# Performance work log

Measured on AMD Instinct MI355X. Metric: run time of the kernel, lower is better.

Reference implementation:

```python
import jax, jax.numpy as jnp
import numpy as np

N_NODES = 100000
N_EDGES = 300000
FEAT = 256
N_GRAPHS = 500
N_LAYERS = 6


def setup_inputs() -> dict:
    key = jax.random.key(0)
    ks = jax.random.split(key, 8)
    x = jax.random.normal(ks[0], (N_NODES, FEAT), dtype=jnp.float32)
    edge_index = jax.random.randint(ks[1], (2, N_EDGES), 0, N_NODES, dtype=jnp.int64)
    batch = jnp.sort(jax.random.randint(ks[2], (N_NODES,), 0, N_GRAPHS, dtype=jnp.int64))
    s = 1.0 / np.sqrt(FEAT)
    # PyG SAGEConv params: lin_l (neighbor path, with bias), lin_r (root path, no bias)
    Wl = jax.random.uniform(ks[3], (N_LAYERS, FEAT, FEAT), jnp.float32, -s, s)
    bl = jax.random.uniform(ks[4], (N_LAYERS, FEAT), jnp.float32, -s, s)
    Wr = jax.random.uniform(ks[5], (N_LAYERS, FEAT, FEAT), jnp.float32, -s, s)
    t = jnp.ones((1,), dtype=jnp.float32)  # SoftmaxAggregation learnable temperature, init 1.0
    return {"x": x, "edge_index": edge_index, "batch": batch,
            "Wl": Wl, "bl": bl, "Wr": Wr, "t": t}


def _sage_conv(x, src, dst, Wl, bl, Wr):
    # mean-aggregate source features onto destinations, then lin_l(agg) + lin_r(x)
    msg_sum = jax.ops.segment_sum(x[src], dst, num_segments=N_NODES)  # [N, F]
    deg = jax.ops.segment_sum(jnp.ones((src.shape[0],), x.dtype), dst, num_segments=N_NODES)
    mean = msg_sum / jnp.maximum(deg, 1.0)[:, None]
    return mean @ Wl.T + bl + x @ Wr.T


def _segment_softmax_aggr(x, batch, t):
    # SoftmaxAggregation: alpha = softmax(t*x over nodes per graph, per feature); out = sum(alpha*x)
    s = t * x  # [N, F]
    m = jax.ops.segment_max(s, batch, num_segments=N_GRAPHS)
    m = jnp.where(jnp.isfinite(m), m, 0.0)  # guard empty segments
    e = jnp.exp(s - m[batch])
    denom = jax.ops.segment_sum(e, batch, num_segments=N_GRAPHS)
    alpha = e / jnp.maximum(denom[batch], 1e-16)
    return jax.ops.segment_sum(alpha * x, batch, num_segments=N_GRAPHS)  # [G, F]


def reference(x, edge_index, batch, Wl, bl, Wr, t):
    src, dst = edge_index[0], edge_index[1]
    for i in range(N_LAYERS):
        x = jax.nn.relu(_sage_conv(x, src, dst, Wl[i], bl[i], Wr[i])) + x
    out = _segment_softmax_aggr(x, batch, t[0])
    return out.reshape(-1, FEAT)
```

## Files before the change

kernel.cpp:

```cpp
#include <hip/hip_runtime.h>
#include <hip/hip_bf16.h>

#define N_NODES  100000
#define N_EDGES  300000
#define FEAT     256
#define N_GRAPHS 500
#define N_LAYERS 6
#define SCAN_B   1024

typedef __attribute__((ext_vector_type(8))) short v8s;
typedef __attribute__((ext_vector_type(4))) float v4f;

__device__ __forceinline__ unsigned short f2bf(float f) {
    unsigned u = __float_as_uint(f);
    unsigned r = u + 0x7fffu + ((u >> 16) & 1u);
    return (unsigned short)(r >> 16);
}
__device__ __forceinline__ float bf2f(unsigned short b) {
    return __uint_as_float(((unsigned)b) << 16);
}

__device__ __forceinline__ void gload16(const ushort* g, ushort* l) {
    __builtin_amdgcn_global_load_lds((const __attribute__((address_space(1))) void*)g,
                                     (__attribute__((address_space(3))) void*)l,
                                     16, 0, 0);
}

__global__ __launch_bounds__(256) void init_kernel(const float* __restrict__ x,
                                                   ushort* __restrict__ xb) {
    int i = blockIdx.x * 256 + threadIdx.x;
    if ((size_t)i * 4 >= (size_t)N_NODES * FEAT) return;
    float4 v = ((const float4*)x)[i];
    ((ushort4*)xb)[i] = make_ushort4(f2bf(v.x), f2bf(v.y), f2bf(v.z), f2bf(v.w));
}

__global__ __launch_bounds__(256) void wconv_kernel(const float* __restrict__ Wl,
                                                    const float* __restrict__ Wr,
                                                    ushort* __restrict__ wlb,
                                                    ushort* __restrict__ wrb) {
    int i = blockIdx.x * 256 + threadIdx.x;
    if ((size_t)i * 4 >= (size_t)N_LAYERS * FEAT * FEAT) return;
    float4 a = ((const float4*)Wl)[i];
    float4 b = ((const float4*)Wr)[i];
    ((ushort4*)wlb)[i] = make_ushort4(f2bf(a.x), f2bf(a.y), f2bf(a.z), f2bf(a.w));
    ((ushort4*)wrb)[i] = make_ushort4(f2bf(b.x), f2bf(b.y), f2bf(b.z), f2bf(b.w));
}


__global__ __launch_bounds__(256) void hist_kernel(const int* __restrict__ dst,
                                                   unsigned* __restrict__ degu) {
    int e = blockIdx.x * 256 + threadIdx.x;
    if (e < N_EDGES) atomicAdd(&degu[dst[e]], 1u);
}

__global__ __launch_bounds__(SCAN_B) void scan_blocks(const unsigned* __restrict__ degu,
                                                      unsigned* __restrict__ excl,
                                                      unsigned* __restrict__ bsum) {
    __shared__ unsigned tmp[SCAN_B];
    int i = blockIdx.x * SCAN_B + threadIdx.x;
    unsigned v = (i < N_NODES) ? degu[i] : 0u;
    tmp[threadIdx.x] = v;
    __syncthreads();
    for (int off = 1; off < SCAN_B; off <<= 1) {
        unsigned add = (threadIdx.x >= off) ? tmp[threadIdx.x - off] : 0u;
        __syncthreads();
        tmp[threadIdx.x] += add;
        __syncthreads();
    }
    if (i < N_NODES) excl[i] = tmp[threadIdx.x] - v;
    if (threadIdx.x == SCAN_B - 1) bsum[blockIdx.x] = tmp[SCAN_B - 1];
}

__global__ void scan_tops(unsigned* __restrict__ bsum, int nb) {
    unsigned run = 0;
    for (int b = 0; b < nb; ++b) { unsigned t = bsum[b]; bsum[b] = run; run += t; }
}

__global__ __launch_bounds__(256) void finalize_rowptr(const unsigned* __restrict__ excl,
                                                       const unsigned* __restrict__ bsum,
                                                       unsigned* __restrict__ rowptr,
                                                       unsigned* __restrict__ cursor) {
    int i = blockIdx.x * 256 + threadIdx.x;
    if (i < N_NODES) {
        unsigned v = excl[i] + bsum[i / SCAN_B];
        rowptr[i] = v;
        cursor[i] = v;
    }
    if (i == N_NODES) rowptr[N_NODES] = N_EDGES;
}

__global__ __launch_bounds__(256) void scatter_kernel(const int* __restrict__ ei,
                                                      unsigned* __restrict__ cursor,
                                                      unsigned* __restrict__ col) {
    int e = blockIdx.x * 256 + threadIdx.x;
    if (e >= N_EDGES) return;
    int d = ei[N_EDGES + e];
    unsigned p = atomicAdd(&cursor[d], 1u);
    col[p] = (unsigned)ei[e];
}

__global__ __launch_bounds__(256) void bounds_kernel(const int* __restrict__ batch,
                                                     unsigned* __restrict__ gs,
                                                     unsigned* __restrict__ ge) {
    int i = blockIdx.x * 256 + threadIdx.x;
    if (i >= N_NODES) return;
    int g = batch[i];
    int gp = (i == 0) ? -1 : batch[i - 1];
    if (g != gp) gs[g] = (unsigned)i;
    int gn = (i == N_NODES - 1) ? -1 : batch[i + 1];
    if (g != gn) ge[g] = (unsigned)(i + 1);
}

__global__ __launch_bounds__(256) void agg_csr(const unsigned* __restrict__ rowptr,
                                               const unsigned* __restrict__ col,
                                               const ushort* __restrict__ xb,
                                               ushort* __restrict__ meanb) {
    int node = blockIdx.x * 4 + (threadIdx.x >> 6);
    int lane = threadIdx.x & 63;
    if (node >= N_NODES) return;
    unsigned s = rowptr[node], e = rowptr[node + 1];
    float a0 = 0.f, a1 = 0.f, a2 = 0.f, a3 = 0.f;
    for (unsigned j = s; j < e; ++j) {
        unsigned src = col[j];
        ushort4 v = *(const ushort4*)(xb + (size_t)src * FEAT + lane * 4);
        a0 += bf2f(v.x); a1 += bf2f(v.y); a2 += bf2f(v.z); a3 += bf2f(v.w);
    }
    float r = 1.0f / fmaxf((float)(e - s), 1.0f);
    ushort4 o = make_ushort4(f2bf(a0 * r), f2bf(a1 * r), f2bf(a2 * r), f2bf(a3 * r));
    *(ushort4*)(meanb + (size_t)node * FEAT + lane * 4) = o;
}

#define ATILE 4096
#define BTILE 8192
#define CPAD  264

__global__ __launch_bounds__(512) void gemm_kernel(const ushort* __restrict__ A0,
                                                   const ushort* __restrict__ A1,
                                                   const ushort* __restrict__ B0,
                                                   const ushort* __restrict__ B1,
                                                   const float* __restrict__ bias,
                                                   ushort* __restrict__ xbn) {
    __shared__ ushort lds[36864];
    ushort (*As)[ATILE] = (ushort(*)[ATILE])lds;
    ushort (*Bs)[BTILE] = (ushort(*)[BTILE])(lds + 3 * ATILE);
    ushort* Cs = lds;

    const int tid  = threadIdx.x;
    const int lane = tid & 63;
    const int wid  = tid >> 6;
    const int wr   = wid >> 2;
    const int wc   = wid & 3;
    const int row0 = blockIdx.x * 128;

    v4f acc[4][4] = {};

    const int fr  = lane & 15;
    const int cbk = (lane >> 4) << 4;

    const int pA  = tid >> 3;
    const int w0A = ((tid & 7) ^ (pA & 7)) << 4;
    int rA = row0 + 2 * pA + (w0A >> 6);
    rA = rA < N_NODES ? rA : N_NODES - 1;
    const int cbA = w0A & 63;
    const int pB0  = tid >> 3;
    const int w0B0 = ((tid & 7) ^ (pB0 & 7)) << 4;
    const int rB0  = 2 * pB0 + (w0B0 >> 6);
    const int cbB0 = w0B0 & 63;
    const int c1   = tid + 512;
    const int pB1  = c1 >> 3;
    const int w0B1 = ((c1 & 7) ^ (pB1 & 7)) << 4;
    const int rB1  = 2 * pB1 + (w0B1 >> 6);
    const int cbB1 = w0B1 & 63;

    #define STAGE(buf, kt) do {                                                   \
        const ushort* Asrc = ((kt) < 8) ? A0 : A1;                                \
        const ushort* Bsrc = ((kt) < 8) ? B0 : B1;                                \
        const int kb = ((kt) & 7) * 32;                                           \
        gload16(Asrc + (size_t)rA  * FEAT + kb + (cbA  >> 1), &As[buf][tid * 8]); \
        gload16(Bsrc + (size_t)rB0 * FEAT + kb + (cbB0 >> 1), &Bs[buf][tid * 8]); \
        gload16(Bsrc + (size_t)rB1 * FEAT + kb + (cbB1 >> 1), &Bs[buf][(size_t)c1 * 8]); \
    } while (0)

    #define FRAG(basePtr, row) \
        (*(const v8s*)((const char*)(basePtr) + (((row) >> 1) * 128 + \
            ((((row) & 1) << 6) + cbk) ^ ((((row) >> 1) & 7) << 4))))

    #define DSREAD(buf) do {                                                      \
        _Pragma("unroll")                                                         \
        for (int i = 0; i < 4; ++i) a[i] = FRAG(As[buf], wr * 64 + i * 16 + fr);  \
        _Pragma("unroll")                                                         \
        for (int j = 0; j < 4; ++j) b[j] = FRAG(Bs[buf], wc * 64 + j * 16 + fr);  \
    } while (0)

    #define MFMA16() do {                                                         \
        _Pragma("unroll")                                                         \
        for (int i = 0; i < 4; ++i)                                               \
            _Pragma("unroll")                                                     \
            for (int j = 0; j < 4; ++j)                                           \
                acc[i][j] = __builtin_amdgcn_mfma_f32_16x16x32_bf16(a[i], b[j], acc[i][j], 0, 0, 0); \
    } while (0)

    STAGE(0, 0);
    STAGE(1, 1);
    int bufC = 0, bufS = 2;
    v8s a[4], b[4];
    #pragma unroll 1
    for (int kt = 0; kt < 15; ++kt) {
        asm volatile("s_waitcnt vmcnt(3)" ::: "memory");
        __builtin_amdgcn_s_barrier();
        __builtin_amdgcn_sched_barrier(0);
        if (kt <= 13) STAGE(bufS, kt + 2);
        DSREAD(bufC);
        asm volatile("s_waitcnt lgkmcnt(0)" ::: "memory");
        __builtin_amdgcn_sched_barrier(0);
        __builtin_amdgcn_s_setprio(1);
        MFMA16();
        __builtin_amdgcn_s_setprio(0);
        bufC = (bufC == 2) ? 0 : bufC + 1;
        bufS = (bufS == 2) ? 0 : bufS + 1;
    }
    asm volatile("s_waitcnt vmcnt(0)" ::: "memory");
    __builtin_amdgcn_s_barrier();
    __builtin_amdgcn_sched_barrier(0);
    DSREAD(bufC);
    asm volatile("s_waitcnt lgkmcnt(0)" ::: "memory");
    __builtin_amdgcn_sched_barrier(0);
    MFMA16();

    __builtin_amdgcn_s_barrier();
    {
        const int orow = (lane >> 4) * 4;
        const int ocol = lane & 15;
        #pragma unroll
        for (int j = 0; j < 4; ++j) {
            int colg = wc * 64 + j * 16 + ocol;
            float bv = bias[colg];
            #pragma unroll
            for (int i = 0; i < 4; ++i) {
                int rl = wr * 64 + i * 16 + orow;
                #pragma unroll
                for (int r = 0; r < 4; ++r)
                    Cs[(rl + r) * CPAD + colg] = f2bf(fmaxf(acc[i][j][r] + bv, 0.0f));
            }
        }
    }
    __builtin_amdgcn_s_barrier();
    #pragma unroll
    for (int p = 0; p < 2; ++p) {
        int rl  = p * 64 + (tid >> 3);
        int row = row0 + rl;
        #pragma unroll
        for (int it = 0; it < 4; ++it) {
            int c0 = (tid & 7) * 8 + it * 64;
            v8s y = *(const v8s*)(Cs + rl * CPAD + c0);
            if (row < N_NODES) {
                v8s xv = *(const v8s*)(A1 + (size_t)row * FEAT + c0);
                v8s o;
                #pragma unroll
                for (int k = 0; k < 8; ++k)
                    o[k] = (short)f2bf(bf2f((ushort)y[k]) + bf2f((ushort)xv[k]));
                *(v8s*)(xbn + (size_t)row * FEAT + c0) = o;
            }
        }
    }
    #undef STAGE
    #undef FRAG
    #undef DSREAD
    #undef MFMA16
}

__global__ __launch_bounds__(512) void smax_kernel(const ushort* __restrict__ xb,
                                                   const unsigned* __restrict__ gs,
                                                   const unsigned* __restrict__ ge,
                                                   const float* __restrict__ t,
                                                   float* __restrict__ out) {
    __shared__ float sm[16 * 256];
    __shared__ float sd[16 * 256];
    __shared__ float sa[16 * 256];
    const int g   = blockIdx.x;
    const unsigned s = gs[g], e = ge[g];
    const float tv2 = t[0] * 1.44269504f;
    const int tid = threadIdx.x;
    const int c   = tid >> 5;
    const int f8  = (tid & 31) * 8;

    float m[8], den[8], acc[8];
    #pragma unroll
    for (int k = 0; k < 8; ++k) { m[k] = -INFINITY; den[k] = 0.f; acc[k] = 0.f; }

    if (s < e) {
        for (unsigned n = s + c; n < e; n += 16) {
            v8s v = *(const v8s*)(xb + (size_t)n * FEAT + f8);
            #pragma unroll
            for (int k = 0; k < 8; ++k) {
                float xv = bf2f((ushort)v[k]);
                float s2 = xv * tv2;
                float mn = fmaxf(m[k], s2);
                float sc = exp2f(m[k] - mn);
                float w  = exp2f(s2 - mn);
                den[k] = den[k] * sc + w;
                acc[k] = acc[k] * sc + w * xv;
                m[k] = mn;
            }
        }
    }
    #pragma unroll
    for (int k = 0; k < 8; ++k) {
        sm[c * 256 + f8 + k] = m[k];
        sd[c * 256 + f8 + k] = den[k];
        sa[c * 256 + f8 + k] = acc[k];
    }
    __syncthreads();
    if (tid < 256) {
        if (s < e) {
            const int f = tid;
            float M = -INFINITY;
            #pragma unroll
            for (int cc = 0; cc < 16; ++cc) M = fmaxf(M, sm[cc * 256 + f]);
            float D = 0.f, A = 0.f;
            #pragma unroll
            for (int cc = 0; cc < 16; ++cc) {
                float w = exp2f(sm[cc * 256 + f] - M);
                D += sd[cc * 256 + f] * w;
                A += sa[cc * 256 + f] * w;
            }
            out[(size_t)g * FEAT + tid] = A / fmaxf(D, 1e-16f);
        } else {
            out[(size_t)g * FEAT + tid] = 0.f;
        }
    }
}

extern "C" void kernel_launch(void* const* d_in, const int* in_sizes, int n_in,
                              void* d_out, int out_size, void* d_ws, size_t ws_size,
                              hipStream_t stream) {
    const float* x     = (const float*)d_in[0];
    const int*   ei    = (const int*)d_in[1];
    const int*   batch = (const int*)d_in[2];
    const float* Wl    = (const float*)d_in[3];
    const float* bl    = (const float*)d_in[4];
    const float* Wr    = (const float*)d_in[5];
    const float* t     = (const float*)d_in[6];
    float* out = (float*)d_out;

    const size_t NF2 = (size_t)N_NODES * FEAT * 2;
    const size_t WSZ = (size_t)N_LAYERS * FEAT * FEAT * 2;

    char* ws = (char*)d_ws;
    size_t off = 0;
    ushort* xb0   = (ushort*)(ws + off); off += NF2;
    ushort* xb1   = (ushort*)(ws + off); off += NF2;
    ushort* meanb = (ushort*)(ws + off); off += NF2;
    ushort* wlb   = (ushort*)(ws + off); off += WSZ;
    ushort* wrb   = (ushort*)(ws + off); off += WSZ;
    unsigned* degu   = (unsigned*)(ws + off); off += (size_t)N_NODES * 4;
    unsigned* excl   = (unsigned*)(ws + off); off += (size_t)N_NODES * 4;
    unsigned* bsum   = (unsigned*)(ws + off); off += 128 * 4;
    unsigned* rowptr = (unsigned*)(ws + off); off += (size_t)(N_NODES + 1) * 4;
    unsigned* cursor = (unsigned*)(ws + off); off += (size_t)N_NODES * 4;
    unsigned* col    = (unsigned*)(ws + off); off += (size_t)N_EDGES * 4;
    unsigned* gs     = (unsigned*)(ws + off); off += (size_t)N_GRAPHS * 4;
    unsigned* ge     = (unsigned*)(ws + off); off += (size_t)N_GRAPHS * 4;

    hipMemsetAsync(degu, 0, (size_t)N_NODES * 4, stream);
    hipMemsetAsync(gs, 0xFF, (size_t)N_GRAPHS * 4, stream);
    hipMemsetAsync(ge, 0, (size_t)N_GRAPHS * 4, stream);

    init_kernel<<<(N_NODES * FEAT / 4 + 255) / 256, 256, 0, stream>>>(x, xb0);
    wconv_kernel<<<(N_LAYERS * FEAT * FEAT / 4 + 255) / 256, 256, 0, stream>>>(Wl, Wr, wlb, wrb);

    const int NB_SCAN = (N_NODES + SCAN_B - 1) / SCAN_B;
    hist_kernel<<<(N_EDGES + 255) / 256, 256, 0, stream>>>(ei + N_EDGES, degu);
    scan_blocks<<<NB_SCAN, SCAN_B, 0, stream>>>(degu, excl, bsum);
    scan_tops<<<1, 1, 0, stream>>>(bsum, NB_SCAN);
    finalize_rowptr<<<(N_NODES + 256) / 256, 256, 0, stream>>>(excl, bsum, rowptr, cursor);
    scatter_kernel<<<(N_EDGES + 255) / 256, 256, 0, stream>>>(ei, cursor, col);

    bounds_kernel<<<(N_NODES + 255) / 256, 256, 0, stream>>>(batch, gs, ge);

    ushort* cur = xb0;
    ushort* nxt = xb1;
    for (int l = 0; l < N_LAYERS; ++l) {
        agg_csr<<<(N_NODES + 3) / 4, 256, 0, stream>>>(rowptr, col, cur, meanb);
        gemm_kernel<<<dim3((N_NODES + 127) / 128), 512, 0, stream>>>(
            meanb, cur,
            wlb + (size_t)l * FEAT * FEAT, wrb + (size_t)l * FEAT * FEAT,
            bl + (size_t)l * FEAT, nxt);
        ushort* tmp = cur; cur = nxt; nxt = tmp;
    }

    smax_kernel<<<N_GRAPHS, 512, 0, stream>>>(cur, gs, ge, t, out);
}
```

Baseline: 666.0 us.

## Fuse CSR mean aggregation into the SAGE GEMM kernel with 64-row tiles

The separate agg_csr kernel and the meanb buffer are removed. Each GEMM block now gathers neighbor means for its 64 rows straight into LDS, with lanes sharing column indices by shuffle, and then runs the MFMA K-loop reading A from LDS for the mean half and streaming X for the root half. This drops one launch per layer and a full bf16 N×F write and read of the mean matrix. In exchange the tile shrinks to 64 rows, B traffic per row doubles, the pipeline moves to simpler double buffering with __syncthreads each step, and the irregular gather now sits inside the GEMM before any MFMA work can start.

```diff
diff --git a/kernel.cpp b/kernel.cpp
--- a/kernel.cpp
+++ b/kernel.cpp
@@ -111,57 +111,29 @@
     if (g != gn) ge[g] = (unsigned)(i + 1);
 }
 
-__global__ __launch_bounds__(256) void agg_csr(const unsigned* __restrict__ rowptr,
-                                               const unsigned* __restrict__ col,
-                                               const ushort* __restrict__ xb,
-                                               ushort* __restrict__ meanb) {
-    int node = blockIdx.x * 4 + (threadIdx.x >> 6);
-    int lane = threadIdx.x & 63;
-    if (node >= N_NODES) return;
-    unsigned s = rowptr[node], e = rowptr[node + 1];
-    float a0 = 0.f, a1 = 0.f, a2 = 0.f, a3 = 0.f;
-    for (unsigned j = s; j < e; ++j) {
-        unsigned src = col[j];
-        ushort4 v = *(const ushort4*)(xb + (size_t)src * FEAT + lane * 4);
-        a0 += bf2f(v.x); a1 += bf2f(v.y); a2 += bf2f(v.z); a3 += bf2f(v.w);
-    }
-    float r = 1.0f / fmaxf((float)(e - s), 1.0f);
-    ushort4 o = make_ushort4(f2bf(a0 * r), f2bf(a1 * r), f2bf(a2 * r), f2bf(a3 * r));
-    *(ushort4*)(meanb + (size_t)node * FEAT + lane * 4) = o;
-}
-
-#define ATILE 4096
-#define BTILE 8192
 #define CPAD  264
 
-__global__ __launch_bounds__(512) void gemm_kernel(const ushort* __restrict__ A0,
-                                                   const ushort* __restrict__ A1,
-                                                   const ushort* __restrict__ B0,
-                                                   const ushort* __restrict__ B1,
-                                                   const float* __restrict__ bias,
-                                                   ushort* __restrict__ xbn) {
+__global__ __launch_bounds__(512, 4) void gemm_kernel(
+        const unsigned* __restrict__ rowptr,
+        const unsigned* __restrict__ col,
+        const ushort* __restrict__ xb,
+        const ushort* __restrict__ B0,
+        const ushort* __restrict__ B1,
+        const float*  __restrict__ bias,
+        ushort* __restrict__ xbn) {
     __shared__ ushort lds[36864];
-    ushort (*As)[ATILE] = (ushort(*)[ATILE])lds;
-    ushort (*Bs)[BTILE] = (ushort(*)[BTILE])(lds + 3 * ATILE);
-    ushort* Cs = lds;
+    ushort* Ms  = lds;
+    ushort* Bs0 = lds + 16384;
+    ushort* Bs1 = lds + 24576;
+    ushort* Xs0 = lds + 32768;
+    ushort* Xs1 = lds + 34816;
+    ushort* Cs  = lds;
 
     const int tid  = threadIdx.x;
     const int lane = tid & 63;
     const int wid  = tid >> 6;
-    const int wr   = wid >> 2;
-    const int wc   = wid & 3;
-    const int row0 = blockIdx.x * 128;
-
-    v4f acc[4][4] = {};
-
-    const int fr  = lane & 15;
-    const int cbk = (lane >> 4) << 4;
-
-    const int pA  = tid >> 3;
-    const int w0A = ((tid & 7) ^ (pA & 7)) << 4;
-    int rA = row0 + 2 * pA + (w0A >> 6);
-    rA = rA < N_NODES ? rA : N_NODES - 1;
-    const int cbA = w0A & 63;
+    const int row0 = blockIdx.x * 64;
+
     const int pB0  = tid >> 3;
     const int w0B0 = ((tid & 7) ^ (pB0 & 7)) << 4;
     const int rB0  = 2 * pB0 + (w0B0 >> 6);
@@ -171,73 +143,122 @@
     const int w0B1 = ((c1 & 7) ^ (pB1 & 7)) << 4;
     const int rB1  = 2 * pB1 + (w0B1 >> 6);
     const int cbB1 = w0B1 & 63;
-
-    #define STAGE(buf, kt) do {                                                   \
-        const ushort* Asrc = ((kt) < 8) ? A0 : A1;                                \
+    const int pX   = tid >> 3;
+    const int w0X  = ((tid & 7) ^ (pX & 7)) << 4;
+    int rX = row0 + 2 * pX + (w0X >> 6);
+    rX = rX < N_NODES ? rX : N_NODES - 1;
+    const int cbX  = w0X & 63;
+
+    #define STAGE_B(bufPtr, kt) do {                                              \
         const ushort* Bsrc = ((kt) < 8) ? B0 : B1;                                \
         const int kb = ((kt) & 7) * 32;                                           \
-        gload16(Asrc + (size_t)rA  * FEAT + kb + (cbA  >> 1), &As[buf][tid * 8]); \
-        gload16(Bsrc + (size_t)rB0 * FEAT + kb + (cbB0 >> 1), &Bs[buf][tid * 8]); \
-        gload16(Bsrc + (size_t)rB1 * FEAT + kb + (cbB1 >> 1), &Bs[buf][(size_t)c1 * 8]); \
+        gload16(Bsrc + (size_t)rB0 * FEAT + kb + (cbB0 >> 1), (bufPtr) + tid * 8);\
+        gload16(Bsrc + (size_t)rB1 * FEAT + kb + (cbB1 >> 1), (bufPtr) + (size_t)c1 * 8); \
     } while (0)
+
+    #define STAGE_X(bufPtr, kt) do {                                              \
+        if (tid < 256) {                                                          \
+            const int kb = ((kt) & 7) * 32;                                       \
+            gload16(xb + (size_t)rX * FEAT + kb + (cbX >> 1), (bufPtr) + tid * 8);\
+        }                                                                          \
+    } while (0)
+
+    STAGE_B(Bs0, 0);
+
+    {
+        const int h   = lane >> 5;
+        const int l32 = lane & 31;
+        #pragma unroll 1
+        for (int p = 0; p < 4; ++p) {
+            const int nl = wid * 8 + p * 2 + h;
+            const int node = row0 + nl;
+            unsigned s = 0, e = 0;
+            if (node < N_NODES) { s = rowptr[node]; e = rowptr[node + 1]; }
+            float a0=0.f,a1=0.f,a2=0.f,a3=0.f,a4=0.f,a5=0.f,a6=0.f,a7=0.f;
+            #pragma unroll 1
+            for (unsigned base = s; base < e; base += 32) {
+                unsigned idx = base + (unsigned)l32;
+                int cv = (idx < e) ? (int)col[idx] : 0;
+                int n = (int)(e - base); n = n > 32 ? 32 : n;
+                #pragma unroll 1
+                for (int j = 0; j < n; ++j) {
+                    unsigned src = (unsigned)__shfl(cv, (h << 5) + j);
+                    v8s v = *(const v8s*)(xb + (size_t)src * FEAT + l32 * 8);
+                    a0 += bf2f((ushort)v[0]); a1 += bf2f((ushort)v[1]);
+                    a2 += bf2f((ushort)v[2]); a3 += bf2f((ushort)v[3]);
+                    a4 += bf2f((ushort)v[4]); a5 += bf2f((ushort)v[5]);
+                    a6 += bf2f((ushort)v[6]); a7 += bf2f((ushort)v[7]);
+                }
+            }
+            float r = 1.0f / fmaxf((float)(e - s), 1.0f);
+            v8s o;
+            o[0]=(short)f2bf(a0*r); o[1]=(short)f2bf(a1*r);
+            o[2]=(short)f2bf(a2*r); o[3]=(short)f2bf(a3*r);
+            o[4]=(short)f2bf(a4*r); o[5]=(short)f2bf(a5*r);
+            o[6]=(short)f2bf(a6*r); o[7]=(short)f2bf(a7*r);
+            *(v8s*)((char*)Ms + nl * 512 + ((l32 * 16) ^ ((nl & 7) << 4))) = o;
+        }
+    }
+    __syncthreads();
+
+    v4f acc[4][2] = {};
+    const int fr  = lane & 15;
+    const int cbk = (lane >> 4) << 4;
 
     #define FRAG(basePtr, row) \
         (*(const v8s*)((const char*)(basePtr) + (((row) >> 1) * 128 + \
             ((((row) & 1) << 6) + cbk) ^ ((((row) >> 1) & 7) << 4))))
 
-    #define DSREAD(buf) do {                                                      \
+    #define AFRAG_M(kt, row) \
+        (*(const v8s*)((const char*)Ms + (row) * 512 + \
+            ((((kt) << 6) + cbk) ^ (((row) & 7) << 4))))
+
+    #define PHASE(kt, APART) do {                                                 \
+        v8s a[4], b[2];                                                           \
         _Pragma("unroll")                                                         \
-        for (int i = 0; i < 4; ++i) a[i] = FRAG(As[buf], wr * 64 + i * 16 + fr);  \
-        _Pragma("unroll")                                                         \
-        for (int j = 0; j < 4; ++j) b[j] = FRAG(Bs[buf], wc * 64 + j * 16 + fr);  \
-    } while (0)
-
-    #define MFMA16() do {                                                         \
+        for (int i = 0; i < 4; ++i) a[i] = APART;                                 \
+        {                                                                          \
+            const ushort* bp = ((kt) & 1) ? Bs1 : Bs0;                            \
+            _Pragma("unroll")                                                     \
+            for (int j = 0; j < 2; ++j) b[j] = FRAG(bp, wid * 32 + j * 16 + fr);  \
+        }                                                                          \
         _Pragma("unroll")                                                         \
         for (int i = 0; i < 4; ++i)                                               \
             _Pragma("unroll")                                                     \
-            for (int j = 0; j < 4; ++j)                                           \
+            for (int j = 0; j < 2; ++j)                                           \
                 acc[i][j] = __builtin_amdgcn_mfma_f32_16x16x32_bf16(a[i], b[j], acc[i][j], 0, 0, 0); \
     } while (0)
 
-    STAGE(0, 0);
-    STAGE(1, 1);
-    int bufC = 0, bufS = 2;
-    v8s a[4], b[4];
-    #pragma unroll 1
-    for (int kt = 0; kt < 15; ++kt) {
-        asm volatile("s_waitcnt vmcnt(3)" ::: "memory");
-        __builtin_amdgcn_s_barrier();
-        __builtin_amdgcn_sched_barrier(0);
-        if (kt <= 13) STAGE(bufS, kt + 2);
-        DSREAD(bufC);
-        asm volatile("s_waitcnt lgkmcnt(0)" ::: "memory");
-        __builtin_amdgcn_sched_barrier(0);
-        __builtin_amdgcn_s_setprio(1);
-        MFMA16();
-        __builtin_amdgcn_s_setprio(0);
-        bufC = (bufC == 2) ? 0 : bufC + 1;
-        bufS = (bufS == 2) ? 0 : bufS + 1;
-    }
-    asm volatile("s_waitcnt vmcnt(0)" ::: "memory");
-    __builtin_amdgcn_s_barrier();
-    __builtin_amdgcn_sched_barrier(0);
-    DSREAD(bufC);
-    asm volatile("s_waitcnt lgkmcnt(0)" ::: "memory");
-    __builtin_amdgcn_sched_barrier(0);
-    MFMA16();
-
-    __builtin_amdgcn_s_barrier();
+    #pragma unroll
+    for (int kt = 0; kt < 8; ++kt) {
+        STAGE_B((kt & 1) ? Bs0 : Bs1, kt + 1);
+        if (kt == 7) STAGE_X(Xs0, 8);
+        PHASE(kt, AFRAG_M(kt, i * 16 + fr));
+        __syncthreads();
+    }
+    #pragma unroll
+    for (int kt = 8; kt < 16; ++kt) {
+        if (kt < 15) {
+            STAGE_B((kt & 1) ? Bs0 : Bs1, kt + 1);
+            STAGE_X((kt & 1) ? Xs0 : Xs1, kt + 1);
+        }
+        const ushort* xp = (kt & 1) ? Xs1 : Xs0;
+        PHASE(kt, FRAG(xp, i * 16 + fr));
+        __syncthreads();
+    }
+    #undef PHASE
+    #undef AFRAG_M
+
     {
         const int orow = (lane >> 4) * 4;
         const int ocol = lane & 15;
         #pragma unroll
-        for (int j = 0; j < 4; ++j) {
-            int colg = wc * 64 + j * 16 + ocol;
+        for (int j = 0; j < 2; ++j) {
+            int colg = wid * 32 + j * 16 + ocol;
             float bv = bias[colg];
             #pragma unroll
             for (int i = 0; i < 4; ++i) {
-                int rl = wr * 64 + i * 16 + orow;
+                int rl = i * 16 + orow;
                 #pragma unroll
                 for (int r = 0; r < 4; ++r)
                     Cs[(rl + r) * CPAD + colg] = f2bf(fmaxf(acc[i][j][r] + bv, 0.0f));
@@ -245,16 +266,15 @@
         }
     }
     __builtin_amdgcn_s_barrier();
-    #pragma unroll
-    for (int p = 0; p < 2; ++p) {
-        int rl  = p * 64 + (tid >> 3);
+    {
+        int rl  = tid >> 3;
         int row = row0 + rl;
         #pragma unroll
         for (int it = 0; it < 4; ++it) {
             int c0 = (tid & 7) * 8 + it * 64;
             v8s y = *(const v8s*)(Cs + rl * CPAD + c0);
             if (row < N_NODES) {
-                v8s xv = *(const v8s*)(A1 + (size_t)row * FEAT + c0);
+                v8s xv = *(const v8s*)(xb + (size_t)row * FEAT + c0);
                 v8s o;
                 #pragma unroll
                 for (int k = 0; k < 8; ++k)
@@ -263,10 +283,9 @@
             }
         }
     }
-    #undef STAGE
+    #undef STAGE_B
+    #undef STAGE_X
     #undef FRAG
-    #undef DSREAD
-    #undef MFMA16
 }
 
 __global__ __launch_bounds__(512) void smax_kernel(const ushort* __restrict__ xb,
@@ -350,7 +369,6 @@
     size_t off = 0;
     ushort* xb0   = (ushort*)(ws + off); off += NF2;
     ushort* xb1   = (ushort*)(ws + off); off += NF2;
-    ushort* meanb = (ushort*)(ws + off); off += NF2;
     ushort* wlb   = (ushort*)(ws + off); off += WSZ;
     ushort* wrb   = (ushort*)(ws + off); off += WSZ;
     unsigned* degu   = (unsigned*)(ws + off); off += (size_t)N_NODES * 4;
@@ -381,9 +399,8 @@
     ushort* cur = xb0;
     ushort* nxt = xb1;
     for (int l = 0; l < N_LAYERS; ++l) {
-        agg_csr<<<(N_NODES + 3) / 4, 256, 0, stream>>>(rowptr, col, cur, meanb);
-        gemm_kernel<<<dim3((N_NODES + 127) / 128), 512, 0, stream>>>(
-            meanb, cur,
+        gemm_kernel<<<dim3((N_NODES + 63) / 64), 512, 0, stream>>>(
+            rowptr, col, cur,
             wlb + (size_t)l * FEAT * FEAT, wrb + (size_t)l * FEAT * FEAT,
             bl + (size_t)l * FEAT, nxt);
         ushort* tmp = cur; cur = nxt; nxt = tmp;
```

Result: faster. 605.5 us (-9.1%).
